# Performance work log

Hardware: AMD Instinct MI355X
Metric: run time of the kernel (lower is better)

The kernel has to match this reference:

```python
import jax, jax.numpy as jnp
import numpy as np

B, N, D, K = 4, 4096, 128, 20

def setup_inputs() -> dict:
    key = jax.random.key(0)
    k1, k2, k3 = jax.random.split(key, 3)
    s = 1.0 / np.sqrt(D)
    return {
        "x": jax.random.normal(k1, (B, N, D), dtype=jnp.float32),
        "Wq": jax.random.normal(k2, (D, D), dtype=jnp.float32) * s,
        "bq": jnp.zeros((D,), dtype=jnp.float32),
        "Wk": jax.random.normal(k3, (D, D), dtype=jnp.float32) * s,
        "bk": jnp.zeros((D,), dtype=jnp.float32),
    }

def reference(x, Wq, bq, Wk, bk):
    # Q/K projections: [B,N,D]
    Q = jnp.einsum('bnd,de->bne', x, Wq) + bq
    Kp = jnp.einsum('bnd,de->bne', x, Wk) + bk
    # scores: [B,N,N], scaled by sqrt(D)
    attn = jnp.einsum('bnd,bmd->bnm', Q, Kp) / jnp.sqrt(jnp.float32(D))
    # top-k along last dim -> binary mask via scatter
    _, topk_idx = jax.lax.top_k(attn, K)  # [B,N,K]
    bi = jnp.arange(B)[:, None, None]
    ni = jnp.arange(N)[None, :, None]
    mask = jnp.zeros_like(attn).at[bi, ni, topk_idx].set(1.0)
    # zero out non-topk entries, then full softmax over all N (zeros included,
    # matching the torch module exactly)
    sparse_attn = attn * mask
    out = jax.nn.softmax(sparse_attn, axis=-1)
    return out[..., None]  # [B,N,N,1]
```

## Files before the change

### kernel.cpp

```cpp
#include <hip/hip_runtime.h>

#define BN 4096
#define BD 128
#define NB 4
#define TOPK 20
#define CAND 96
#define EPS_U 0.9f

typedef float f32x16 __attribute__((ext_vector_type(16)));
typedef short bf16x8 __attribute__((ext_vector_type(8)));

__device__ inline unsigned short f2bf(float f) {
  unsigned int u = __float_as_uint(f);
  unsigned int r = (u + 0x7FFFu + ((u >> 16) & 1u)) >> 16;
  return (unsigned short)r;
}

__global__ __launch_bounds__(256) void proj_kernel(
    const float* __restrict__ x,
    const float* __restrict__ Wq, const float* __restrict__ bq,
    const float* __restrict__ Wk, const float* __restrict__ bk,
    double* __restrict__ Qd, double* __restrict__ Kd, unsigned short* __restrict__ Khi) {
  __shared__ double xs[32][129];
  const int tid = threadIdx.x;
  const long row0 = (long)blockIdx.x * 32;
  const float* xsrc = x + row0 * BD;
  for (int i = tid; i < 32 * BD; i += 256) xs[i >> 7][i & 127] = (double)xsrc[i];
  __syncthreads();

  const int e = tid & 127;
  const bool isK = tid >= 128;
  const float* W = isK ? Wk : Wq;
  const float* bias = isK ? bk : bq;
  double* Od = isK ? Kd : Qd;

  double acc[32];
  const double binit = (double)bias[e];
#pragma unroll
  for (int r = 0; r < 32; ++r) acc[r] = binit;

  for (int d = 0; d < BD; ++d) {
    const double wv = (double)W[d * BD + e];
#pragma unroll
    for (int r = 0; r < 32; ++r) acc[r] = fma(xs[r][d], wv, acc[r]);
  }

#pragma unroll
  for (int r = 0; r < 32; ++r) {
    const double a = acc[r];
    const long o = (row0 + r) * BD + e;
    Od[o] = a;
    if (isK) Khi[o] = f2bf((float)a);
  }
}

__global__ __launch_bounds__(512) void screen_kernel(
    const double* __restrict__ Qd, const unsigned short* __restrict__ Khi,
    unsigned short* __restrict__ Sbf) {
  __shared__ char sbuf[8][2560];

  const int tid = threadIdx.x;
  const int lane = tid & 63;
  const int w = tid >> 6;
  const int kt = w & 3, qt = w >> 2;
  const int c31 = lane & 31, hi = lane >> 5;

  const int blk = blockIdx.x;
  const int xcd = blk & 7;
  const int j = blk >> 3;
  const int combo = xcd * 2 + (j & 1);
  const int b = combo >> 2;
  const int kq = combo & 3;
  const int rg = j >> 1;
  const int rowbase = rg << 6;
  const int kvbase = kq << 10;

  const int qrow = qt * 32 + c31;
  const long grow = (long)b * BN + rowbase + qrow;

  bf16x8 bqf[8];
  {
    const double* qp = Qd + grow * BD + hi * 8;
#pragma unroll
    for (int ks = 0; ks < 8; ++ks) {
      bf16x8 pk;
#pragma unroll
      for (int jj = 0; jj < 8; ++jj) pk[jj] = (short)f2bf((float)qp[ks * 16 + jj]);
      bqf[ks] = pk;
    }
  }

  const unsigned short* kb = Khi + ((long)b * BN + kvbase + kt * 32 + c31) * BD + hi * 8;
  char* my = sbuf[w];
  const int wr = c31 * 80;

  const long gq = (long)b * BN + rowbase + qt * 32 + (lane >> 1);
  unsigned short* dstbase = Sbf + gq * BN + kvbase + kt * 32 + (lane & 1) * 16;
  const char* rdp = my + (lane >> 1) * 80 + (lane & 1) * 32;

  for (int step = 0; step < 8; ++step) {
    const unsigned short* kr = kb + (long)step * 128 * BD;
    f32x16 acc = {0.f, 0.f, 0.f, 0.f, 0.f, 0.f, 0.f, 0.f,
                  0.f, 0.f, 0.f, 0.f, 0.f, 0.f, 0.f, 0.f};
#pragma unroll
    for (int ks = 0; ks < 8; ++ks) {
      const bf16x8 a = *(const bf16x8*)(kr + ks * 16);
      acc = __builtin_amdgcn_mfma_f32_32x32x16_bf16(a, bqf[ks], acc, 0, 0, 0);
    }

#pragma unroll
    for (int p = 0; p < 4; ++p) {
      const unsigned int lo =
          (unsigned int)f2bf(acc[p * 4 + 0]) | ((unsigned int)f2bf(acc[p * 4 + 1]) << 16);
      const unsigned int hi2 =
          (unsigned int)f2bf(acc[p * 4 + 2]) | ((unsigned int)f2bf(acc[p * 4 + 3]) << 16);
      *(uint2*)(my + wr + p * 16 + hi * 8) = make_uint2(lo, hi2);
    }
    const uint4 r0 = *(const uint4*)(rdp);
    const uint4 r1 = *(const uint4*)(rdp + 16);
    unsigned short* dst = dstbase + step * 128;
    *(uint4*)dst = r0;
    *(uint4*)(dst + 8) = r1;
  }
}

__device__ inline float rescore_f64(const double2* __restrict__ kp2, const double2* __restrict__ q2) {
  double a0 = 0.0, a1 = 0.0, a2 = 0.0, a3 = 0.0;
#pragma unroll
  for (int i = 0; i < 64; i += 4) {
    a0 = fma(q2[i + 0].y, kp2[i + 0].y, fma(q2[i + 0].x, kp2[i + 0].x, a0));
    a1 = fma(q2[i + 1].y, kp2[i + 1].y, fma(q2[i + 1].x, kp2[i + 1].x, a1));
    a2 = fma(q2[i + 2].y, kp2[i + 2].y, fma(q2[i + 2].x, kp2[i + 2].x, a2));
    a3 = fma(q2[i + 3].y, kp2[i + 3].y, fma(q2[i + 3].x, kp2[i + 3].x, a3));
  }
  return (float)(((a0 + a1) + (a2 + a3)) * 8.8388347648318447e-02);
}

__device__ inline unsigned int fmono(float v) {
  const unsigned int u = __float_as_uint(v);
  return (u & 0x80000000u) ? ~u : (u | 0x80000000u);
}
__device__ inline float fdemono(unsigned int k) {
  const unsigned int u = (k & 0x80000000u) ? (k & 0x7fffffffu) : ~k;
  return __uint_as_float(u);
}

__global__ __launch_bounds__(256) void topk_kernel(
    const double* __restrict__ Qd, const double* __restrict__ Kd,
    const unsigned short* __restrict__ Sbf, unsigned int* __restrict__ rec) {
  __shared__ unsigned short listL[4][CAND];
  __shared__ unsigned int cntL[4];

  const int tid = threadIdx.x;
  const int lane = tid & 63;
  const int w = tid >> 6;
  const int blk = blockIdx.x;
  const int b = (blk & 7) >> 1;
  const int idx = ((blk >> 3) << 1) | (blk & 1);
  const long row = (long)b * BN + idx * 4 + w;

  const unsigned short* srow = Sbf + row * BN;

  uint4 v[8];
  float pm[8];
#pragma unroll
  for (int i = 0; i < 8; ++i) {
    v[i] = *(const uint4*)(srow + i * 512 + lane * 8);
    float m0 = -3.4e38f;
#pragma unroll
    for (int k = 0; k < 4; ++k) {
      const unsigned int u = (&v[i].x)[k];
      m0 = fmaxf(m0, fmaxf(__uint_as_float(u << 16), __uint_as_float(u & 0xFFFF0000u)));
    }
    pm[i] = m0;
  }
  float mymax = fmaxf(fmaxf(fmaxf(pm[0], pm[1]), fmaxf(pm[2], pm[3])),
                      fmaxf(fmaxf(pm[4], pm[5]), fmaxf(pm[6], pm[7])));

  float vb = mymax;
#pragma unroll
  for (int k = 2; k <= 64; k <<= 1) {
#pragma unroll
    for (int jj = k >> 1; jj > 0; jj >>= 1) {
      const float o = __shfl_xor(vb, jj);
      const bool keepmin = (((lane & k) == 0) == ((lane & jj) == 0));
      vb = keepmin ? fminf(vb, o) : fmaxf(vb, o);
    }
  }
  const float th = __shfl(vb, 44) - EPS_U;

  if (lane == 0) cntL[w] = 0;

#pragma unroll
  for (int i = 0; i < 8; ++i) {
#pragma unroll
    for (int k = 0; k < 4; ++k) {
      const unsigned int u = (&v[i].x)[k];
      const float f0 = __uint_as_float(u << 16);
      const float f1 = __uint_as_float(u & 0xFFFF0000u);
      const int col0 = i * 512 + lane * 8 + k * 2;
      if (f0 >= th) {
        const unsigned int p = atomicAdd(&cntL[w], 1u);
        if (p < CAND) listL[w][p] = (unsigned short)col0;
      }
      if (f1 >= th) {
        const unsigned int p = atomicAdd(&cntL[w], 1u);
        if (p < CAND) listL[w][p] = (unsigned short)(col0 + 1);
      }
    }
  }

  const int c = (int)min(cntL[w], (unsigned int)CAND);

  const double2* q2 = (const double2*)(Qd + row * BD);
  const double* kbd = Kd + (long)b * BN * BD;

  unsigned long long key0 = 0ull, key1 = 0ull;
  if (lane < c) {
    const int kv = (int)listL[w][lane];
    const float vv = rescore_f64((const double2*)(kbd + (long)kv * BD), q2);
    key0 = ((unsigned long long)fmono(vv) << 12) | (unsigned int)(4095 - kv);
  }
  if (lane + 64 < c) {
    const int kv = (int)listL[w][lane + 64];
    const float vv = rescore_f64((const double2*)(kbd + (long)kv * BD), q2);
    key1 = ((unsigned long long)fmono(vv) << 12) | (unsigned int)(4095 - kv);
  }

  unsigned int* rr = rec + row * 48;

  if (c <= 64) {
    unsigned long long kk = key0;
#pragma unroll
    for (int k = 2; k <= 64; k <<= 1) {
#pragma unroll
      for (int jj = k >> 1; jj > 0; jj >>= 1) {
        const unsigned long long o = __shfl_xor(kk, jj);
        const bool keepmin = (((lane & k) == 0) == ((lane & jj) == 0));
        kk = keepmin ? (o < kk ? o : kk) : (o > kk ? o : kk);
      }
    }
    const unsigned long long ktop = __shfl(kk, 63);
    const float m = fmaxf(fdemono((unsigned int)(ktop >> 12)), 0.0f);
    const float val = fdemono((unsigned int)(kk >> 12));
    const int col = 4095 - (int)(kk & 0xFFFull);
    const float e = (lane >= 44) ? expf(val - m) : 0.0f;
    float se = e;
#pragma unroll
    for (int off = 32; off; off >>= 1) se += __shfl_xor(se, off);
    const float Z = se + (float)(BN - TOPK) * expf(-m);
    if (lane >= 44) {
      const int r = 63 - lane;
      rr[r] = __float_as_uint(e / Z);
      rr[20 + r] = (unsigned int)col;
    }
    if (lane == 0) rr[40] = __float_as_uint(expf(-m) / Z);
  } else {
    if (key1 > key0) { const unsigned long long t = key0; key0 = key1; key1 = t; }
    float m = 0.0f, se = 0.0f;
    float myval = 0.0f;
    int mycol = 0;
    for (int it = 0; it < TOPK; ++it) {
      unsigned long long rk = key0;
      for (int off = 32; off; off >>= 1) {
        const unsigned long long ok = __shfl_xor(rk, off);
        rk = (ok > rk) ? ok : rk;
      }
      const float rv = fdemono((unsigned int)(rk >> 12));
      if (it == 0) m = fmaxf(rv, 0.0f);
      se += expf(rv - m);
      if (lane == it) { myval = rv; mycol = 4095 - (int)(rk & 0xFFFull); }
      if (key0 == rk) { key0 = key1; key1 = 0ull; }
    }
    const float Z = se + (float)(BN - TOPK) * expf(-m);
    if (lane < TOPK) {
      rr[lane] = __float_as_uint(expf(myval - m) / Z);
      rr[20 + lane] = (unsigned int)mycol;
    }
    if (lane == 0) rr[40] = __float_as_uint(expf(-m) / Z);
  }
}

__global__ __launch_bounds__(256) void fill_kernel(
    const unsigned int* __restrict__ rec, float* __restrict__ out) {
  __shared__ unsigned int bm[128];
  __shared__ float pv[TOPK];
  __shared__ int pc[TOPK];
  __shared__ float sc0;

  const int tid = threadIdx.x;
  const long row = blockIdx.x;
  const unsigned int* rr = rec + row * 48;

  if (tid < 128) bm[tid] = 0;
  __syncthreads();
  if (tid < TOPK) {
    pv[tid] = __uint_as_float(rr[tid]);
    const int col = (int)rr[20 + tid];
    pc[tid] = col;
    atomicOr(&bm[col >> 5], 1u << (col & 31));
  }
  if (tid == TOPK) sc0 = __uint_as_float(rr[40]);
  __syncthreads();

  const float c0 = sc0;
  const float4 cv = make_float4(c0, c0, c0, c0);
  float4* op = (float4*)(out + row * BN);

#pragma unroll
  for (int k = 0; k < 4; ++k) {
    const int j = tid + k * 256;
    const unsigned int bits = (bm[j >> 3] >> ((j & 7) * 4)) & 0xFu;
    if (bits == 0u) {
      op[j] = cv;
    } else {
      float4 v = cv;
      const int col0 = j * 4;
#pragma unroll
      for (int cmp = 0; cmp < 4; ++cmp) {
        if ((bits >> cmp) & 1u) {
          const int col = col0 + cmp;
          float pvv = c0;
          for (int i = 0; i < TOPK; ++i)
            if (pc[i] == col) pvv = pv[i];
          (&v.x)[cmp] = pvv;
        }
      }
      op[j] = v;
    }
  }
}

extern "C" void kernel_launch(void* const* d_in, const int* in_sizes, int n_in,
                              void* d_out, int out_size, void* d_ws, size_t ws_size,
                              hipStream_t stream) {
  const float* x  = (const float*)d_in[0];
  const float* Wq = (const float*)d_in[1];
  const float* bq = (const float*)d_in[2];
  const float* Wk = (const float*)d_in[3];
  const float* bk = (const float*)d_in[4];
  float* out = (float*)d_out;

  const long NE = (long)NB * BN * BD;
  const long NR = (long)NB * BN;
  double* Qd = (double*)d_ws;
  double* Kd = Qd + NE;
  unsigned short* Khi = (unsigned short*)(Kd + NE);
  unsigned short* Sbf = Khi + NE;
  unsigned int* rec = (unsigned int*)(Sbf + NR * BN);

  proj_kernel<<<NB * BN / 32, 256, 0, stream>>>(x, Wq, bq, Wk, bk, Qd, Kd, Khi);
  screen_kernel<<<1024, 512, 0, stream>>>(Qd, Khi, Sbf);
  topk_kernel<<<NR / 4, 256, 0, stream>>>(Qd, Kd, Sbf, rec);
  fill_kernel<<<NR, 256, 0, stream>>>(rec, out);
}
```

Before: 326.0 us.

## Stage K tiles in swizzled LDS and replace bitonic sorts with rank counting

In the screening kernel, each K chunk is now loaded cooperatively into a 32KB XOR-swizzled shared-memory buffer, with the next chunk prefetched into registers while the current one is used. This replaces direct per-lane global fragment loads and adds two block barriers per step. In the top-k kernel, the bitonic sort used for the threshold and the final ranking becomes a 64-step shuffle rank count, and the LDS atomic compaction becomes ballot plus popcount prefix sums. The shuffle loops may cost more instructions than the bitonic networks they replace.

Measured after the change: 344.6 us. +5.7%, slower.

```diff
diff --git a/kernel.cpp b/kernel.cpp
--- a/kernel.cpp
+++ b/kernel.cpp
@@ -57,6 +57,7 @@
 __global__ __launch_bounds__(512) void screen_kernel(
     const double* __restrict__ Qd, const unsigned short* __restrict__ Khi,
     unsigned short* __restrict__ Sbf) {
+  __shared__ char kbuf[32768];
   __shared__ char sbuf[8][2560];
 
   const int tid = threadIdx.x;
@@ -90,21 +91,48 @@
     }
   }
 
-  const unsigned short* kb = Khi + ((long)b * BN + kvbase + kt * 32 + c31) * BD + hi * 8;
+  const char* kb = (const char*)(Khi + ((long)b * BN + kvbase) * BD);
+  const int ar = kt * 32 + c31;
+  const int ar256 = ar * 256;
+  const int arx = ar & 15;
+
   char* my = sbuf[w];
   const int wr = c31 * 80;
-
   const long gq = (long)b * BN + rowbase + qt * 32 + (lane >> 1);
   unsigned short* dstbase = Sbf + gq * BN + kvbase + kt * 32 + (lane & 1) * 16;
   const char* rdp = my + (lane >> 1) * 80 + (lane & 1) * 32;
 
+  uint4 stg[4];
+#define LOADSTG(s)                                                \
+  {                                                               \
+    const char* gsrc_ = kb + (long)(s)*32768 + tid * 16;          \
+    stg[0] = *(const uint4*)(gsrc_);                              \
+    stg[1] = *(const uint4*)(gsrc_ + 8192);                       \
+    stg[2] = *(const uint4*)(gsrc_ + 16384);                      \
+    stg[3] = *(const uint4*)(gsrc_ + 24576);                      \
+  }
+#define WRITESTG()                                                \
+  {                                                               \
+    _Pragma("unroll") for (int j_ = 0; j_ < 4; ++j_) {            \
+      const int L_ = j_ * 8192 + tid * 16;                        \
+      const int r_ = L_ >> 8;                                     \
+      const int c_ = (L_ >> 4) & 15;                              \
+      *(uint4*)(kbuf + r_ * 256 + ((c_ ^ (r_ & 15)) << 4)) = stg[j_]; \
+    }                                                             \
+  }
+
+  LOADSTG(0);
+  WRITESTG();
+  __syncthreads();
+
   for (int step = 0; step < 8; ++step) {
-    const unsigned short* kr = kb + (long)step * 128 * BD;
+    if (step < 7) LOADSTG(step + 1);
+
     f32x16 acc = {0.f, 0.f, 0.f, 0.f, 0.f, 0.f, 0.f, 0.f,
                   0.f, 0.f, 0.f, 0.f, 0.f, 0.f, 0.f, 0.f};
 #pragma unroll
     for (int ks = 0; ks < 8; ++ks) {
-      const bf16x8 a = *(const bf16x8*)(kr + ks * 16);
+      const bf16x8 a = *(const bf16x8*)(kbuf + ar256 + (((ks * 2 + hi) ^ arx) << 4));
       acc = __builtin_amdgcn_mfma_f32_32x32x16_bf16(a, bqf[ks], acc, 0, 0, 0);
     }
 
@@ -116,12 +144,20 @@
           (unsigned int)f2bf(acc[p * 4 + 2]) | ((unsigned int)f2bf(acc[p * 4 + 3]) << 16);
       *(uint2*)(my + wr + p * 16 + hi * 8) = make_uint2(lo, hi2);
     }
-    const uint4 r0 = *(const uint4*)(rdp);
-    const uint4 r1 = *(const uint4*)(rdp + 16);
-    unsigned short* dst = dstbase + step * 128;
-    *(uint4*)dst = r0;
-    *(uint4*)(dst + 8) = r1;
-  }
+    {
+      const uint4 r0 = *(const uint4*)(rdp);
+      const uint4 r1 = *(const uint4*)(rdp + 16);
+      unsigned short* dst = dstbase + step * 128;
+      *(uint4*)dst = r0;
+      *(uint4*)(dst + 8) = r1;
+    }
+
+    __syncthreads();
+    if (step < 7) WRITESTG();
+    __syncthreads();
+  }
+#undef LOADSTG
+#undef WRITESTG
 }
 
 __device__ inline float rescore_f64(const double2* __restrict__ kp2, const double2* __restrict__ q2) {
@@ -149,7 +185,6 @@
     const double* __restrict__ Qd, const double* __restrict__ Kd,
     const unsigned short* __restrict__ Sbf, unsigned int* __restrict__ rec) {
   __shared__ unsigned short listL[4][CAND];
-  __shared__ unsigned int cntL[4];
 
   const int tid = threadIdx.x;
   const int lane = tid & 63;
@@ -160,6 +195,7 @@
   const long row = (long)b * BN + idx * 4 + w;
 
   const unsigned short* srow = Sbf + row * BN;
+  const unsigned long long lmask = (lane == 63) ? ~0ull >> 1 : (1ull << lane) - 1ull;
 
   uint4 v[8];
   float pm[8];
@@ -174,23 +210,19 @@
     }
     pm[i] = m0;
   }
-  float mymax = fmaxf(fmaxf(fmaxf(pm[0], pm[1]), fmaxf(pm[2], pm[3])),
-                      fmaxf(fmaxf(pm[4], pm[5]), fmaxf(pm[6], pm[7])));
-
-  float vb = mymax;
-#pragma unroll
-  for (int k = 2; k <= 64; k <<= 1) {
-#pragma unroll
-    for (int jj = k >> 1; jj > 0; jj >>= 1) {
-      const float o = __shfl_xor(vb, jj);
-      const bool keepmin = (((lane & k) == 0) == ((lane & jj) == 0));
-      vb = keepmin ? fminf(vb, o) : fmaxf(vb, o);
-    }
-  }
-  const float th = __shfl(vb, 44) - EPS_U;
-
-  if (lane == 0) cntL[w] = 0;
-
+  const float mymax = fmaxf(fmaxf(fmaxf(pm[0], pm[1]), fmaxf(pm[2], pm[3])),
+                            fmaxf(fmaxf(pm[4], pm[5]), fmaxf(pm[6], pm[7])));
+
+  int trank = 0;
+  for (int j2 = 0; j2 < 64; ++j2) {
+    const float ov = __shfl(mymax, j2);
+    trank += (ov > mymax || (ov == mymax && j2 < lane)) ? 1 : 0;
+  }
+  const unsigned long long m19 = __ballot(trank == 19);
+  const float tau = __shfl(mymax, (int)(__ffsll((long long)m19) - 1));
+  const float th = tau - EPS_U;
+
+  unsigned int base = 0;
 #pragma unroll
   for (int i = 0; i < 8; ++i) {
 #pragma unroll
@@ -199,18 +231,21 @@
       const float f0 = __uint_as_float(u << 16);
       const float f1 = __uint_as_float(u & 0xFFFF0000u);
       const int col0 = i * 512 + lane * 8 + k * 2;
+      const unsigned long long b0 = __ballot(f0 >= th);
       if (f0 >= th) {
-        const unsigned int p = atomicAdd(&cntL[w], 1u);
+        const unsigned int p = base + (unsigned int)__popcll(b0 & lmask);
         if (p < CAND) listL[w][p] = (unsigned short)col0;
       }
+      base += (unsigned int)__popcll(b0);
+      const unsigned long long b1 = __ballot(f1 >= th);
       if (f1 >= th) {
-        const unsigned int p = atomicAdd(&cntL[w], 1u);
+        const unsigned int p = base + (unsigned int)__popcll(b1 & lmask);
         if (p < CAND) listL[w][p] = (unsigned short)(col0 + 1);
       }
-    }
-  }
-
-  const int c = (int)min(cntL[w], (unsigned int)CAND);
+      base += (unsigned int)__popcll(b1);
+    }
+  }
+  const int c = (int)min(base, (unsigned int)CAND);
 
   const double2* q2 = (const double2*)(Qd + row * BD);
   const double* kbd = Kd + (long)b * BN * BD;
@@ -230,29 +265,24 @@
   unsigned int* rr = rec + row * 48;
 
   if (c <= 64) {
-    unsigned long long kk = key0;
-#pragma unroll
-    for (int k = 2; k <= 64; k <<= 1) {
-#pragma unroll
-      for (int jj = k >> 1; jj > 0; jj >>= 1) {
-        const unsigned long long o = __shfl_xor(kk, jj);
-        const bool keepmin = (((lane & k) == 0) == ((lane & jj) == 0));
-        kk = keepmin ? (o < kk ? o : kk) : (o > kk ? o : kk);
-      }
-    }
-    const unsigned long long ktop = __shfl(kk, 63);
-    const float m = fmaxf(fdemono((unsigned int)(ktop >> 12)), 0.0f);
-    const float val = fdemono((unsigned int)(kk >> 12));
-    const int col = 4095 - (int)(kk & 0xFFFull);
-    const float e = (lane >= 44) ? expf(val - m) : 0.0f;
+    int krank = 0;
+    for (int j2 = 0; j2 < 64; ++j2) {
+      const unsigned long long ok = __shfl(key0, j2);
+      krank += (ok > key0) ? 1 : 0;
+    }
+    const unsigned long long mm = __ballot(krank == 0);
+    const unsigned long long mkey = __shfl(key0, (int)(__ffsll((long long)mm) - 1));
+    const float m = fmaxf(fdemono((unsigned int)(mkey >> 12)), 0.0f);
+
+    const float val = fdemono((unsigned int)(key0 >> 12));
+    const float e = (krank < TOPK) ? expf(val - m) : 0.0f;
     float se = e;
 #pragma unroll
     for (int off = 32; off; off >>= 1) se += __shfl_xor(se, off);
     const float Z = se + (float)(BN - TOPK) * expf(-m);
-    if (lane >= 44) {
-      const int r = 63 - lane;
-      rr[r] = __float_as_uint(e / Z);
-      rr[20 + r] = (unsigned int)col;
+    if (krank < TOPK) {
+      rr[krank] = __float_as_uint(e / Z);
+      rr[20 + krank] = (unsigned int)(4095 - (int)(key0 & 0xFFFull));
     }
     if (lane == 0) rr[40] = __float_as_uint(expf(-m) / Z);
   } else {
```
